# Performance work log

Measured on AMD Instinct MI355X. Metric: run time of the kernel, lower is better.

The kernel has to match this reference:

```python
import jax, jax.numpy as jnp
import numpy as np

NEG_SLOPE = 0.2
EPS = 1e-16


def _add_self_loops(edge_index, num_nodes):
    loop = jnp.arange(num_nodes, dtype=edge_index.dtype)
    return jnp.concatenate([edge_index, jnp.stack([loop, loop])], axis=1)


def gat_conv(x, edge_index, W, a_src, a_dst, b, concat):
    """PyG-style GATConv: gather -> attention logits -> segment softmax -> scatter-add."""
    N = x.shape[0]
    H, C = a_src.shape
    xl = (x @ W).reshape(N, H, C)                       # [N,H,C]
    alpha_src = (xl * a_src[None]).sum(-1)              # [N,H]
    alpha_dst = (xl * a_dst[None]).sum(-1)              # [N,H]
    src, dst = edge_index[0], edge_index[1]
    alpha = jax.nn.leaky_relu(alpha_src[src] + alpha_dst[dst], NEG_SLOPE)  # [E,H]
    amax = jax.ops.segment_max(alpha, dst, num_segments=N)
    amax = jnp.where(jnp.isfinite(amax), amax, 0.0)
    ea = jnp.exp(alpha - amax[dst])
    denom = jax.ops.segment_sum(ea, dst, num_segments=N)
    attn = ea / (denom[dst] + EPS)                      # [E,H]
    msg = xl[src] * attn[:, :, None]                    # [E,H,C]
    out = jax.ops.segment_sum(msg, dst, num_segments=N)  # [N,H,C]
    out = out.reshape(N, H * C) if concat else out.mean(axis=1)
    return out + b


def setup_inputs() -> dict:
    key = jax.random.key(0)
    ks = jax.random.split(key, 9)
    N, F, E, H, C, NC = 100000, 128, 1600000, 8, 8, 40
    s = lambda fan: 1.0 / np.sqrt(fan)
    return {
        "x": jax.random.normal(ks[0], (N, F), dtype=jnp.float32),
        "edge_index": jax.random.randint(ks[1], (2, E), 0, N, dtype=jnp.int64),
        "W1": jax.random.normal(ks[2], (F, H * C), dtype=jnp.float32) * s(F),
        "a_src1": jax.random.normal(ks[3], (H, C), dtype=jnp.float32) * s(C),
        "a_dst1": jax.random.normal(ks[4], (H, C), dtype=jnp.float32) * s(C),
        "b1": jnp.zeros((H * C,), dtype=jnp.float32),
        "W2": jax.random.normal(ks[5], (H * C, NC), dtype=jnp.float32) * s(H * C),
        "a_src2": jax.random.normal(ks[6], (1, NC), dtype=jnp.float32) * s(NC),
        "a_dst2": jax.random.normal(ks[7], (1, NC), dtype=jnp.float32) * s(NC),
        "b2": jnp.zeros((NC,), dtype=jnp.float32),
    }


def reference(x, edge_index, W1, a_src1, a_dst1, b1, W2, a_src2, a_dst2, b2):
    N = x.shape[0]
    ei = _add_self_loops(edge_index, N)
    h = gat_conv(x, ei, W1, a_src1, a_dst1, b1, concat=True)   # [N,64]
    h = jax.nn.elu(h)
    out = gat_conv(h, ei, W2, a_src2, a_dst2, b2, concat=True)  # [N,nclass]
    return out
```

## Files before the change

kernel.cpp:

```cpp
#include <hip/hip_runtime.h>
#include <math.h>

#define NEG_SLOPE 0.2f
#define GAT_EPS 1e-16f
#define LOG2E 1.44269504088896340736f

#define CH   2048
#define NBK  512
#define MAXCH 864

__device__ __forceinline__ unsigned pack_bf16(float a, float b) {
    unsigned ua = __float_as_uint(a);
    unsigned ub = __float_as_uint(b);
    ua = (ua + 0x8000u) >> 16;
    ub = (ub + 0x8000u) & 0xffff0000u;
    return ua | ub;
}
__device__ __forceinline__ float bf_lo(unsigned pk) {
    return __uint_as_float(pk << 16);
}
__device__ __forceinline__ float bf_hi(unsigned pk) {
    return __uint_as_float(pk & 0xffff0000u);
}


__global__ __launch_bounds__(256) void k_off_a(
    const int* __restrict__ cnt, int* __restrict__ off,
    int* __restrict__ tot, int NCHv)
{
    __shared__ int st[8][MAXCH];
    __shared__ int psum[8][33];
    int b0 = blockIdx.x * 8;
    int t = threadIdx.x;
    for (int idx = t; idx < NCHv * 8; idx += 256) {
        int bl = idx & 7, c = idx >> 3;
        st[bl][c] = cnt[(size_t)c * NBK + b0 + bl];
    }
    __syncthreads();
    int bl = t >> 5, j = t & 31;
    int per = (NCHv + 31) / 32;
    int cbeg = j * per;
    int cend = min(cbeg + per, NCHv);
    int s = 0;
    for (int c = cbeg; c < cend; c++) s += st[bl][c];
    psum[bl][j] = s;
    __syncthreads();
    if (j == 0) {
        int run = 0;
        for (int k = 0; k < 32; k++) { int v = psum[bl][k]; psum[bl][k] = run; run += v; }
        psum[bl][32] = run;
    }
    __syncthreads();
    int run = psum[bl][j];
    for (int c = cbeg; c < cend; c++) { int v = st[bl][c]; st[bl][c] = run; run += v; }
    __syncthreads();
    for (int idx = t; idx < NCHv * 8; idx += 256) {
        int blw = idx & 7, c = idx >> 3;
        off[(size_t)c * NBK + b0 + blw] = st[blw][c];
    }
    if (j == 0) tot[b0 + bl] = psum[bl][32];
}

__global__ __launch_bounds__(256) void k_place(
    const int* __restrict__ ei, int E, int N, int shift,
    const int* __restrict__ off, const int* __restrict__ tot,
    unsigned* __restrict__ bslab)
{
    __shared__ int cur[NBK];
    __shared__ int ps[256];
    int c = blockIdx.x;
    int t = threadIdx.x;
    int carry = 0;
    for (int b0 = 0; b0 < NBK; b0 += 256) {
        int v = tot[b0 + t];
        ps[t] = v;
        __syncthreads();
        for (int o = 1; o < 256; o <<= 1) {
            int u = (t >= o) ? ps[t - o] : 0;
            __syncthreads();
            ps[t] += u;
            __syncthreads();
        }
        cur[b0 + t] = carry + ps[t] - v + off[(size_t)c * NBK + b0 + t];
        carry += ps[255];
        __syncthreads();
    }
    __syncthreads();

    int Etot = E + N;
    int base = c * CH;
    int lim = min(base + CH, Etot);
    int mask = (1 << shift) - 1;
    for (int e = base + t; e < lim; e += 256) {
        int s, d;
        if (e < E) { s = ei[e]; d = ei[E + e]; }
        else       { s = e - E; d = s; }
        int b = d >> shift;
        int pos = atomicAdd(&cur[b], 1);
        bslab[pos] = (unsigned)s | ((unsigned)(d & mask) << 17);
    }
}

__global__ __launch_bounds__(256) void k_csr2(
    const int* __restrict__ tot, const unsigned* __restrict__ bslab,
    int shift, int* __restrict__ row_ptr, int* __restrict__ csr_src,
    int N, int Etot)
{
    __shared__ int sdeg[1024];
    __shared__ int scur[1024];
    __shared__ int ps[256];
    __shared__ int bb[NBK + 1];
    int b = blockIdx.x;
    int tid = threadIdx.x;

    int carry = 0;
    for (int b0 = 0; b0 < NBK; b0 += 256) {
        int v = tot[b0 + tid];
        ps[tid] = v;
        __syncthreads();
        for (int o = 1; o < 256; o <<= 1) {
            int u = (tid >= o) ? ps[tid - o] : 0;
            __syncthreads();
            ps[tid] += u;
            __syncthreads();
        }
        bb[b0 + tid] = carry + ps[tid] - v;
        carry += ps[255];
        __syncthreads();
    }
    if (tid == 0) bb[NBK] = carry;
    __syncthreads();

    int beg = bb[b], end = bb[b + 1];
    int nodes = 1 << shift;
    int node0 = b << shift;
    for (int i = tid; i < nodes; i += 256) sdeg[i] = 0;
    __syncthreads();
    for (int i = beg + tid; i < end; i += 256)
        atomicAdd(&sdeg[bslab[i] >> 17], 1);
    __syncthreads();
    int per = (nodes + 255) / 256;
    int mybase = tid * per;
    int sum = 0;
    for (int j = 0; j < per; j++) sum += sdeg[mybase + j];
    ps[tid] = sum;
    __syncthreads();
    int v0 = ps[tid];
    for (int o = 1; o < 256; o <<= 1) {
        int v = (tid >= o) ? ps[tid - o] : 0;
        __syncthreads();
        ps[tid] += v;
        __syncthreads();
    }
    int run = ps[tid] - v0;
    for (int j = 0; j < per; j++) {
        int i = mybase + j;
        int dgi = sdeg[i];
        scur[i] = beg + run;
        int node = node0 + i;
        if (node < N) row_ptr[node] = beg + run;
        run += dgi;
    }
    if (b == 0 && tid == 0) row_ptr[N] = Etot;
    __syncthreads();
    for (int i = beg + tid; i < end; i += 256) {
        unsigned w = bslab[i];
        int pos = atomicAdd(&scur[w >> 17], 1);
        csr_src[pos] = (int)(w & 0x1FFFFu);
    }
}

__device__ __forceinline__ void emit_node1(
    const float* acc, int n, int q, int c0,
    const float* asrc, const float* adst,
    unsigned* __restrict__ xl1b, float* __restrict__ as1,
    float* __restrict__ ad1)
{
    uint4 pk0, pk1;
    pk0.x = pack_bf16(acc[0], acc[1]);  pk0.y = pack_bf16(acc[2], acc[3]);
    pk0.z = pack_bf16(acc[4], acc[5]);  pk0.w = pack_bf16(acc[6], acc[7]);
    pk1.x = pack_bf16(acc[8], acc[9]);  pk1.y = pack_bf16(acc[10], acc[11]);
    pk1.z = pack_bf16(acc[12], acc[13]); pk1.w = pack_bf16(acc[14], acc[15]);
    uint4* xo = (uint4*)(xl1b + (size_t)n * 32 + q * 8);
    xo[0] = pk0;
    xo[1] = pk1;
#pragma unroll
    for (int hh = 0; hh < 2; hh++) {
        float s = 0.0f, t = 0.0f;
#pragma unroll
        for (int c = 0; c < 8; c++) {
            s = fmaf(acc[hh * 8 + c], asrc[c0 + hh * 8 + c], s);
            t = fmaf(acc[hh * 8 + c], adst[c0 + hh * 8 + c], t);
        }
        as1[(size_t)n * 8 + 2 * q + hh] = s * LOG2E;
        ad1[(size_t)n * 8 + 2 * q + hh] = t * LOG2E;
    }
}

__global__ __launch_bounds__(256) void k_gemm1(
    const float* __restrict__ x, const float* __restrict__ W1,
    const float* __restrict__ a_src1, const float* __restrict__ a_dst1,
    unsigned* __restrict__ xl1b, float* __restrict__ as1,
    float* __restrict__ ad1, int N, int F,
    const int* __restrict__ ei, int E, int shift, int NCHv,
    int* __restrict__ cnt)
{
    __shared__ float Ws[128 * 64];
    __shared__ float asrc[64];
    __shared__ float adst[64];
    __shared__ int hist[NBK];

    if (blockIdx.x < NCHv) {
        for (int i = threadIdx.x; i < NBK; i += 256) hist[i] = 0;
        __syncthreads();
        int Etot = E + N;
        int base = blockIdx.x * CH;
        int lim = min(base + CH, Etot);
        for (int e = base + threadIdx.x; e < lim; e += 256) {
            int d = (e < E) ? ei[E + e] : (e - E);
            atomicAdd(&hist[d >> shift], 1);
        }
        __syncthreads();
        for (int i = threadIdx.x; i < NBK; i += 256)
            cnt[(size_t)blockIdx.x * NBK + i] = hist[i];
    }
    if (blockIdx.x * 256 >= N) return;

    for (int i = threadIdx.x; i < F * 64; i += 256) Ws[i] = W1[i];
    if (threadIdx.x < 64) {
        asrc[threadIdx.x] = a_src1[threadIdx.x];
        adst[threadIdx.x] = a_dst1[threadIdx.x];
    }
    __syncthreads();

    int q = threadIdx.x & 3;
    int n0 = blockIdx.x * 256 + (threadIdx.x >> 2) * 4;
    if (n0 >= N) return;
    int c0 = q * 16;
    int n1 = min(n0 + 1, N - 1);
    int n2 = min(n0 + 2, N - 1);
    int n3 = min(n0 + 3, N - 1);

    float acc0[16], acc1[16], acc2[16], acc3[16];
#pragma unroll
    for (int c = 0; c < 16; c++) { acc0[c]=0.f; acc1[c]=0.f; acc2[c]=0.f; acc3[c]=0.f; }

    const float4* xr0 = (const float4*)(x + (size_t)n0 * F);
    const float4* xr1 = (const float4*)(x + (size_t)n1 * F);
    const float4* xr2 = (const float4*)(x + (size_t)n2 * F);
    const float4* xr3 = (const float4*)(x + (size_t)n3 * F);

#define GEMM1_ROW(comp, ridx)                                        \
    { const float* w = &Ws[(k4 * 4 + ridx) * 64 + c0];               \
      _Pragma("unroll")                                              \
      for (int c = 0; c < 16; c++) {                                 \
          float wc = w[c];                                           \
          acc0[c] = fmaf(xv0.comp, wc, acc0[c]);                     \
          acc1[c] = fmaf(xv1.comp, wc, acc1[c]);                     \
          acc2[c] = fmaf(xv2.comp, wc, acc2[c]);                     \
          acc3[c] = fmaf(xv3.comp, wc, acc3[c]); } }

    int K4 = F / 4;
    float4 xv0 = xr0[0], xv1 = xr1[0], xv2 = xr2[0], xv3 = xr3[0];
    float4 nx0 = xr0[1], nx1 = xr1[1], nx2 = xr2[1], nx3 = xr3[1];
    for (int k4 = 0; k4 < K4; k4++) {
        float4 fx0 = xv0, fx1 = xv1, fx2 = xv2, fx3 = xv3;
        int kn = k4 + 2;
        if (kn < K4) { fx0 = xr0[kn]; fx1 = xr1[kn]; fx2 = xr2[kn]; fx3 = xr3[kn]; }
        GEMM1_ROW(x, 0)
        GEMM1_ROW(y, 1)
        GEMM1_ROW(z, 2)
        GEMM1_ROW(w, 3)
        xv0 = nx0; xv1 = nx1; xv2 = nx2; xv3 = nx3;
        nx0 = fx0; nx1 = fx1; nx2 = fx2; nx3 = fx3;
    }
#undef GEMM1_ROW

    emit_node1(acc0, n0, q, c0, asrc, adst, xl1b, as1, ad1);
    if (n0 + 1 < N) emit_node1(acc1, n0 + 1, q, c0, asrc, adst, xl1b, as1, ad1);
    if (n0 + 2 < N) emit_node1(acc2, n0 + 2, q, c0, asrc, adst, xl1b, as1, ad1);
    if (n0 + 3 < N) emit_node1(acc3, n0 + 3, q, c0, asrc, adst, xl1b, as1, ad1);
}

__global__ __launch_bounds__(256) void k_agg1(
    const int* __restrict__ row_ptr, const int* __restrict__ csr_src,
    const float* __restrict__ as1, const float* __restrict__ ad1,
    const unsigned* __restrict__ xl1b, const float* __restrict__ b1,
    float* __restrict__ h1, int d0, int dend)
{
    int d = d0 + blockIdx.x * 8 + ((threadIdx.x >> 6) << 1) + ((threadIdx.x >> 5) & 1);
    if (d >= dend) return;
    int lane = threadIdx.x & 31;
    int g = lane >> 3;
    int l = lane & 7;

    int beg = row_ptr[d], end = row_ptr[d + 1];
    float adh = ad1[(size_t)d * 8 + l];

    float ax[8];
#pragma unroll
    for (int j = 0; j < 8; j++) ax[j] = 0.f;
    float den = 0.f;

    int i = beg + g;
    for (; i + 4 < end; i += 8) {
        int s0 = csr_src[i];
        int s1 = csr_src[i + 4];
        size_t q0 = (size_t)s0 * 8 + l;
        size_t q1 = (size_t)s1 * 8 + l;
        float al0 = as1[q0] + adh;
        float al1 = as1[q1] + adh;
        uint4 k0 = *(const uint4*)(xl1b + (q0 << 2));
        uint4 k1 = *(const uint4*)(xl1b + (q1 << 2));
        al0 = fmaxf(al0, NEG_SLOPE * al0);
        al1 = fmaxf(al1, NEG_SLOPE * al1);
        float e0 = __builtin_amdgcn_exp2f(al0);
        float e1 = __builtin_amdgcn_exp2f(al1);
        ax[0] = fmaf(e0, bf_lo(k0.x), ax[0]);
        ax[1] = fmaf(e0, bf_hi(k0.x), ax[1]);
        ax[2] = fmaf(e0, bf_lo(k0.y), ax[2]);
        ax[3] = fmaf(e0, bf_hi(k0.y), ax[3]);
        ax[4] = fmaf(e0, bf_lo(k0.z), ax[4]);
        ax[5] = fmaf(e0, bf_hi(k0.z), ax[5]);
        ax[6] = fmaf(e0, bf_lo(k0.w), ax[6]);
        ax[7] = fmaf(e0, bf_hi(k0.w), ax[7]);
        ax[0] = fmaf(e1, bf_lo(k1.x), ax[0]);
        ax[1] = fmaf(e1, bf_hi(k1.x), ax[1]);
        ax[2] = fmaf(e1, bf_lo(k1.y), ax[2]);
        ax[3] = fmaf(e1, bf_hi(k1.y), ax[3]);
        ax[4] = fmaf(e1, bf_lo(k1.z), ax[4]);
        ax[5] = fmaf(e1, bf_hi(k1.z), ax[5]);
        ax[6] = fmaf(e1, bf_lo(k1.w), ax[6]);
        ax[7] = fmaf(e1, bf_hi(k1.w), ax[7]);
        den += e0 + e1;
    }
    if (i < end) {
        int s0 = csr_src[i];
        size_t q0 = (size_t)s0 * 8 + l;
        float al0 = as1[q0] + adh;
        uint4 k0 = *(const uint4*)(xl1b + (q0 << 2));
        al0 = fmaxf(al0, NEG_SLOPE * al0);
        float e0 = __builtin_amdgcn_exp2f(al0);
        ax[0] = fmaf(e0, bf_lo(k0.x), ax[0]);
        ax[1] = fmaf(e0, bf_hi(k0.x), ax[1]);
        ax[2] = fmaf(e0, bf_lo(k0.y), ax[2]);
        ax[3] = fmaf(e0, bf_hi(k0.y), ax[3]);
        ax[4] = fmaf(e0, bf_lo(k0.z), ax[4]);
        ax[5] = fmaf(e0, bf_hi(k0.z), ax[5]);
        ax[6] = fmaf(e0, bf_lo(k0.w), ax[6]);
        ax[7] = fmaf(e0, bf_hi(k0.w), ax[7]);
        den += e0;
    }

#pragma unroll
    for (int m = 8; m < 32; m <<= 1) {
#pragma unroll
        for (int j = 0; j < 8; j++) ax[j] += __shfl_xor(ax[j], m);
        den += __shfl_xor(den, m);
    }

    if (g == 0) {
        float inv = __builtin_amdgcn_rcpf(den + GAT_EPS);
        const float4* bb = (const float4*)(b1 + l * 8);
        float4 b0 = bb[0], b1v = bb[1];
        float4 o0, o1;
        float v;
        v = fmaf(ax[0], inv, b0.x);  o0.x = v > 0.f ? v : __expf(v) - 1.f;
        v = fmaf(ax[1], inv, b0.y);  o0.y = v > 0.f ? v : __expf(v) - 1.f;
        v = fmaf(ax[2], inv, b0.z);  o0.z = v > 0.f ? v : __expf(v) - 1.f;
        v = fmaf(ax[3], inv, b0.w);  o0.w = v > 0.f ? v : __expf(v) - 1.f;
        v = fmaf(ax[4], inv, b1v.x); o1.x = v > 0.f ? v : __expf(v) - 1.f;
        v = fmaf(ax[5], inv, b1v.y); o1.y = v > 0.f ? v : __expf(v) - 1.f;
        v = fmaf(ax[6], inv, b1v.z); o1.z = v > 0.f ? v : __expf(v) - 1.f;
        v = fmaf(ax[7], inv, b1v.w); o1.w = v > 0.f ? v : __expf(v) - 1.f;
        float4* op = (float4*)(h1 + (size_t)d * 64 + l * 8);
        op[0] = o0;
        op[1] = o1;
    }
}

__global__ __launch_bounds__(256) void k_node2(
    const float* __restrict__ h1, const float* __restrict__ W2,
    const float* __restrict__ a_src2, const float* __restrict__ a_dst2,
    unsigned* __restrict__ xl2b, float* __restrict__ ad2, int N)
{
    __shared__ float Ws[64 * 40];
    __shared__ float a2s[40];
    __shared__ float a2d[40];
    for (int i = threadIdx.x; i < 64 * 40; i += 256) Ws[i] = W2[i];
    if (threadIdx.x < 40) {
        a2s[threadIdx.x] = a_src2[threadIdx.x];
        a2d[threadIdx.x] = a_dst2[threadIdx.x];
    }
    __syncthreads();

    int q = threadIdx.x & 1;
    int n0 = blockIdx.x * 256 + (threadIdx.x >> 1) * 2;
    if (n0 >= N) return;
    int c0 = q * 20;
    int n1 = min(n0 + 1, N - 1);

    float o0[20], o1[20];
#pragma unroll
    for (int j = 0; j < 20; j++) { o0[j] = 0.f; o1[j] = 0.f; }

    const float4* hr0 = (const float4*)(h1 + (size_t)n0 * 64);
    const float4* hr1 = (const float4*)(h1 + (size_t)n1 * 64);

#define NODE2_ROW(comp, ridx)                                        \
    { const float* w = &Ws[(k4 * 4 + ridx) * 40 + c0];               \
      _Pragma("unroll")                                              \
      for (int j = 0; j < 20; j++) {                                 \
          float wj = w[j];                                           \
          o0[j] = fmaf(ha.comp, wj, o0[j]);                          \
          o1[j] = fmaf(hb.comp, wj, o1[j]); } }

    for (int k4 = 0; k4 < 16; k4++) {
        float4 ha = hr0[k4];
        float4 hb = hr1[k4];
        NODE2_ROW(x, 0)
        NODE2_ROW(y, 1)
        NODE2_ROW(z, 2)
        NODE2_ROW(w, 3)
    }
#undef NODE2_ROW

    float s0 = 0.f, t0 = 0.f, s1 = 0.f, t1 = 0.f;
#pragma unroll
    for (int j = 0; j < 20; j++) {
        s0 = fmaf(o0[j], a2s[c0 + j], s0);
        t0 = fmaf(o0[j], a2d[c0 + j], t0);
        s1 = fmaf(o1[j], a2s[c0 + j], s1);
        t1 = fmaf(o1[j], a2d[c0 + j], t1);
    }
    s0 += __shfl_xor(s0, 1);
    t0 += __shfl_xor(t0, 1);
    s1 += __shfl_xor(s1, 1);
    t1 += __shfl_xor(t1, 1);
    if (q == 0) {
        xl2b[(size_t)n0 * 24 + 20] = __float_as_uint(s0 * LOG2E);
        ad2[n0] = t0 * LOG2E;
        if (n0 + 1 < N) {
            xl2b[(size_t)(n0 + 1) * 24 + 20] = __float_as_uint(s1 * LOG2E);
            ad2[n0 + 1] = t1 * LOG2E;
        }
    }

    unsigned* xo0 = xl2b + (size_t)n0 * 24 + q * 10;
#pragma unroll
    for (int p = 0; p < 10; p++) xo0[p] = pack_bf16(o0[2 * p], o0[2 * p + 1]);
    if (n0 + 1 < N) {
        unsigned* xo1 = xl2b + (size_t)(n0 + 1) * 24 + q * 10;
#pragma unroll
        for (int p = 0; p < 10; p++) xo1[p] = pack_bf16(o1[2 * p], o1[2 * p + 1]);
    }
}

__global__ __launch_bounds__(256) void k_agg2(
    const int* __restrict__ row_ptr, const int* __restrict__ csr_src,
    const float* __restrict__ ad2,
    const unsigned* __restrict__ xl2b, const float* __restrict__ b2,
    float* __restrict__ out, int N)
{
    int d = blockIdx.x * 8 + ((threadIdx.x >> 6) << 1) + ((threadIdx.x >> 5) & 1);
    if (d >= N) return;
    int lane = threadIdx.x & 31;
    int g = lane >> 3;
    int l = lane & 7;
    if (l >= 5) return;

    int beg = row_ptr[d], end = row_ptr[d + 1];
    float add = ad2[d];

    float ax[8];
#pragma unroll
    for (int j = 0; j < 8; j++) ax[j] = 0.f;
    float den = 0.f;

    int i = beg + g;
    for (; i + 4 < end; i += 8) {
        int s0 = csr_src[i];
        int s1 = csr_src[i + 4];
        const unsigned* r0 = xl2b + (size_t)s0 * 24;
        const unsigned* r1 = xl2b + (size_t)s1 * 24;
        float al0 = __uint_as_float(r0[20]) + add;
        float al1 = __uint_as_float(r1[20]) + add;
        uint4 k0 = *(const uint4*)(r0 + l * 4);
        uint4 k1 = *(const uint4*)(r1 + l * 4);
        al0 = fmaxf(al0, NEG_SLOPE * al0);
        al1 = fmaxf(al1, NEG_SLOPE * al1);
        float e0 = __builtin_amdgcn_exp2f(al0);
        float e1 = __builtin_amdgcn_exp2f(al1);
        ax[0] = fmaf(e0, bf_lo(k0.x), ax[0]);
        ax[1] = fmaf(e0, bf_hi(k0.x), ax[1]);
        ax[2] = fmaf(e0, bf_lo(k0.y), ax[2]);
        ax[3] = fmaf(e0, bf_hi(k0.y), ax[3]);
        ax[4] = fmaf(e0, bf_lo(k0.z), ax[4]);
        ax[5] = fmaf(e0, bf_hi(k0.z), ax[5]);
        ax[6] = fmaf(e0, bf_lo(k0.w), ax[6]);
        ax[7] = fmaf(e0, bf_hi(k0.w), ax[7]);
        ax[0] = fmaf(e1, bf_lo(k1.x), ax[0]);
        ax[1] = fmaf(e1, bf_hi(k1.x), ax[1]);
        ax[2] = fmaf(e1, bf_lo(k1.y), ax[2]);
        ax[3] = fmaf(e1, bf_hi(k1.y), ax[3]);
        ax[4] = fmaf(e1, bf_lo(k1.z), ax[4]);
        ax[5] = fmaf(e1, bf_hi(k1.z), ax[5]);
        ax[6] = fmaf(e1, bf_lo(k1.w), ax[6]);
        ax[7] = fmaf(e1, bf_hi(k1.w), ax[7]);
        den += e0 + e1;
    }
    if (i < end) {
        int s0 = csr_src[i];
        const unsigned* r0 = xl2b + (size_t)s0 * 24;
        float al0 = __uint_as_float(r0[20]) + add;
        uint4 k0 = *(const uint4*)(r0 + l * 4);
        al0 = fmaxf(al0, NEG_SLOPE * al0);
        float e0 = __builtin_amdgcn_exp2f(al0);
        ax[0] = fmaf(e0, bf_lo(k0.x), ax[0]);
        ax[1] = fmaf(e0, bf_hi(k0.x), ax[1]);
        ax[2] = fmaf(e0, bf_lo(k0.y), ax[2]);
        ax[3] = fmaf(e0, bf_hi(k0.y), ax[3]);
        ax[4] = fmaf(e0, bf_lo(k0.z), ax[4]);
        ax[5] = fmaf(e0, bf_hi(k0.z), ax[5]);
        ax[6] = fmaf(e0, bf_lo(k0.w), ax[6]);
        ax[7] = fmaf(e0, bf_hi(k0.w), ax[7]);
        den += e0;
    }

#pragma unroll
    for (int m = 8; m < 32; m <<= 1) {
#pragma unroll
        for (int j = 0; j < 8; j++) ax[j] += __shfl_xor(ax[j], m);
        den += __shfl_xor(den, m);
    }

    if (g == 0) {
        float inv = __builtin_amdgcn_rcpf(den + GAT_EPS);
        float* op = out + (size_t)d * 40 + l * 8;
        const float* bb = b2 + l * 8;
#pragma unroll
        for (int j = 0; j < 8; j++) op[j] = fmaf(ax[j], inv, bb[j]);
    }
}

extern "C" void kernel_launch(void* const* d_in, const int* in_sizes, int n_in,
                              void* d_out, int out_size, void* d_ws, size_t ws_size,
                              hipStream_t stream) {
    const float* x      = (const float*)d_in[0];
    const int*   ei     = (const int*)d_in[1];
    const float* W1     = (const float*)d_in[2];
    const float* a_src1 = (const float*)d_in[3];
    const float* a_dst1 = (const float*)d_in[4];
    const float* b1     = (const float*)d_in[5];
    const float* W2     = (const float*)d_in[6];
    const float* a_src2 = (const float*)d_in[7];
    const float* a_dst2 = (const float*)d_in[8];
    const float* b2     = (const float*)d_in[9];

    int F = in_sizes[2] / 64;
    int N = in_sizes[0] / F;
    int E = in_sizes[1] / 2;
    int Etot = E + N;
    int NCHv = (Etot + CH - 1) / CH;
    int shift = 8;
    while (((N - 1) >> shift) >= NBK) shift++;

    unsigned* xl1b    = (unsigned*)d_ws;
    float*    h1      = (float*)(xl1b + (size_t)N * 32);
    float*    as1     = h1 + (size_t)N * 64;
    float*    ad1     = as1 + (size_t)N * 8;
    int*      row_ptr = (int*)(ad1 + (size_t)N * 8);
    int*      csr_src = row_ptr + (N + 1);
    unsigned* bslab   = (unsigned*)(csr_src + Etot);
    int*      cnt     = (int*)h1;
    int*      off     = cnt + (size_t)NCHv * NBK;
    int*      tot     = off + (size_t)NCHv * NBK;
    unsigned* xl2b    = xl1b;
    float*    ad2     = ad1;

    int gridG1 = (N + 255) / 256;
    if (gridG1 < NCHv) gridG1 = NCHv;
    k_gemm1<<<gridG1, 256, 0, stream>>>(x, W1, a_src1, a_dst1,
                                        xl1b, as1, ad1, N, F,
                                        ei, E, shift, NCHv, cnt);

    k_off_a<<<NBK / 8, 256, 0, stream>>>(cnt, off, tot, NCHv);
    k_place<<<NCHv, 256, 0, stream>>>(ei, E, N, shift, off, tot, bslab);
    k_csr2 <<<NBK, 256, 0, stream>>>(tot, bslab, shift,
                                     row_ptr, csr_src, N, Etot);

    int N1 = (N / 2) & ~7;
    k_agg1 <<<(N1 + 7) / 8, 256, 0, stream>>>(row_ptr, csr_src, as1, ad1,
                                              xl1b, b1, h1, 0, N1);
    k_agg1 <<<((N - N1) + 7) / 8, 256, 0, stream>>>(row_ptr, csr_src, as1, ad1,
                                                    xl1b, b1, h1, N1, N);

    k_node2<<<(N + 255) / 256, 256, 0, stream>>>(h1, W2, a_src2, a_dst2,
                                                 xl2b, ad2, N);
    k_agg2 <<<(N + 7) / 8, 256, 0, stream>>>(row_ptr, csr_src, ad2,
                                             xl2b, b2, (float*)d_out, N);
}
```

Baseline: 302.5 us.

## Hoist bucket prefix scan into one kernel, shrink GEMM1 per-thread nodes, merge agg1 launches

Adds a single-block k_scan kernel that computes the bucket base offsets once, so k_place and k_csr2 no longer each redo a 512-entry prefix scan in every block. GEMM1 now gives each thread 2 nodes instead of 4, which doubles the grid and lowers register pressure at the cost of more W staging per node. The two split k_agg1 launches are merged into one. This adds one tiny kernel launch but removes repeated scan work and a launch.

```diff
diff --git a/kernel.cpp b/kernel.cpp
--- a/kernel.cpp
+++ b/kernel.cpp
@@ -61,30 +61,34 @@
     if (j == 0) tot[b0 + bl] = psum[bl][32];
 }
 
+__global__ __launch_bounds__(NBK) void k_scan(
+    const int* __restrict__ tot, int* __restrict__ bbase)
+{
+    __shared__ int sm[NBK];
+    int t = threadIdx.x;
+    int v = tot[t];
+    sm[t] = v;
+    __syncthreads();
+    for (int o = 1; o < NBK; o <<= 1) {
+        int u = (t >= o) ? sm[t - o] : 0;
+        __syncthreads();
+        sm[t] += u;
+        __syncthreads();
+    }
+    bbase[t] = sm[t] - v;
+    if (t == NBK - 1) bbase[NBK] = sm[t];
+}
+
 __global__ __launch_bounds__(256) void k_place(
     const int* __restrict__ ei, int E, int N, int shift,
-    const int* __restrict__ off, const int* __restrict__ tot,
+    const int* __restrict__ off, const int* __restrict__ bbase,
     unsigned* __restrict__ bslab)
 {
     __shared__ int cur[NBK];
-    __shared__ int ps[256];
     int c = blockIdx.x;
     int t = threadIdx.x;
-    int carry = 0;
-    for (int b0 = 0; b0 < NBK; b0 += 256) {
-        int v = tot[b0 + t];
-        ps[t] = v;
-        __syncthreads();
-        for (int o = 1; o < 256; o <<= 1) {
-            int u = (t >= o) ? ps[t - o] : 0;
-            __syncthreads();
-            ps[t] += u;
-            __syncthreads();
-        }
-        cur[b0 + t] = carry + ps[t] - v + off[(size_t)c * NBK + b0 + t];
-        carry += ps[255];
-        __syncthreads();
-    }
+    for (int b = t; b < NBK; b += 256)
+        cur[b] = bbase[b] + off[(size_t)c * NBK + b];
     __syncthreads();
 
     int Etot = E + N;
@@ -102,36 +106,16 @@
 }
 
 __global__ __launch_bounds__(256) void k_csr2(
-    const int* __restrict__ tot, const unsigned* __restrict__ bslab,
+    const int* __restrict__ bbase, const unsigned* __restrict__ bslab,
     int shift, int* __restrict__ row_ptr, int* __restrict__ csr_src,
     int N, int Etot)
 {
     __shared__ int sdeg[1024];
     __shared__ int scur[1024];
     __shared__ int ps[256];
-    __shared__ int bb[NBK + 1];
     int b = blockIdx.x;
     int tid = threadIdx.x;
-
-    int carry = 0;
-    for (int b0 = 0; b0 < NBK; b0 += 256) {
-        int v = tot[b0 + tid];
-        ps[tid] = v;
-        __syncthreads();
-        for (int o = 1; o < 256; o <<= 1) {
-            int u = (tid >= o) ? ps[tid - o] : 0;
-            __syncthreads();
-            ps[tid] += u;
-            __syncthreads();
-        }
-        bb[b0 + tid] = carry + ps[tid] - v;
-        carry += ps[255];
-        __syncthreads();
-    }
-    if (tid == 0) bb[NBK] = carry;
-    __syncthreads();
-
-    int beg = bb[b], end = bb[b + 1];
+    int beg = bbase[b], end = bbase[b + 1];
     int nodes = 1 << shift;
     int node0 = b << shift;
     for (int i = tid; i < nodes; i += 256) sdeg[i] = 0;
@@ -224,7 +208,7 @@
         for (int i = threadIdx.x; i < NBK; i += 256)
             cnt[(size_t)blockIdx.x * NBK + i] = hist[i];
     }
-    if (blockIdx.x * 256 >= N) return;
+    if (blockIdx.x * 128 >= N) return;
 
     for (int i = threadIdx.x; i < F * 64; i += 256) Ws[i] = W1[i];
     if (threadIdx.x < 64) {
@@ -234,21 +218,17 @@
     __syncthreads();
 
     int q = threadIdx.x & 3;
-    int n0 = blockIdx.x * 256 + (threadIdx.x >> 2) * 4;
+    int n0 = blockIdx.x * 128 + (threadIdx.x >> 2) * 2;
     if (n0 >= N) return;
     int c0 = q * 16;
     int n1 = min(n0 + 1, N - 1);
-    int n2 = min(n0 + 2, N - 1);
-    int n3 = min(n0 + 3, N - 1);
-
-    float acc0[16], acc1[16], acc2[16], acc3[16];
-#pragma unroll
-    for (int c = 0; c < 16; c++) { acc0[c]=0.f; acc1[c]=0.f; acc2[c]=0.f; acc3[c]=0.f; }
+
+    float acc0[16], acc1[16];
+#pragma unroll
+    for (int c = 0; c < 16; c++) { acc0[c] = 0.f; acc1[c] = 0.f; }
 
     const float4* xr0 = (const float4*)(x + (size_t)n0 * F);
     const float4* xr1 = (const float4*)(x + (size_t)n1 * F);
-    const float4* xr2 = (const float4*)(x + (size_t)n2 * F);
-    const float4* xr3 = (const float4*)(x + (size_t)n3 * F);
 
 #define GEMM1_ROW(comp, ridx)                                        \
     { const float* w = &Ws[(k4 * 4 + ridx) * 64 + c0];               \
@@ -256,40 +236,36 @@
       for (int c = 0; c < 16; c++) {                                 \
           float wc = w[c];                                           \
           acc0[c] = fmaf(xv0.comp, wc, acc0[c]);                     \
-          acc1[c] = fmaf(xv1.comp, wc, acc1[c]);                     \
-          acc2[c] = fmaf(xv2.comp, wc, acc2[c]);                     \
-          acc3[c] = fmaf(xv3.comp, wc, acc3[c]); } }
+          acc1[c] = fmaf(xv1.comp, wc, acc1[c]); } }
 
     int K4 = F / 4;
-    float4 xv0 = xr0[0], xv1 = xr1[0], xv2 = xr2[0], xv3 = xr3[0];
-    float4 nx0 = xr0[1], nx1 = xr1[1], nx2 = xr2[1], nx3 = xr3[1];
+    float4 xv0 = xr0[0], xv1 = xr1[0];
+    float4 nx0 = xr0[1], nx1 = xr1[1];
     for (int k4 = 0; k4 < K4; k4++) {
-        float4 fx0 = xv0, fx1 = xv1, fx2 = xv2, fx3 = xv3;
+        float4 fx0 = xv0, fx1 = xv1;
         int kn = k4 + 2;
-        if (kn < K4) { fx0 = xr0[kn]; fx1 = xr1[kn]; fx2 = xr2[kn]; fx3 = xr3[kn]; }
+        if (kn < K4) { fx0 = xr0[kn]; fx1 = xr1[kn]; }
         GEMM1_ROW(x, 0)
         GEMM1_ROW(y, 1)
         GEMM1_ROW(z, 2)
         GEMM1_ROW(w, 3)
-        xv0 = nx0; xv1 = nx1; xv2 = nx2; xv3 = nx3;
-        nx0 = fx0; nx1 = fx1; nx2 = fx2; nx3 = fx3;
+        xv0 = nx0; xv1 = nx1;
+        nx0 = fx0; nx1 = fx1;
     }
 #undef GEMM1_ROW
 
     emit_node1(acc0, n0, q, c0, asrc, adst, xl1b, as1, ad1);
     if (n0 + 1 < N) emit_node1(acc1, n0 + 1, q, c0, asrc, adst, xl1b, as1, ad1);
-    if (n0 + 2 < N) emit_node1(acc2, n0 + 2, q, c0, asrc, adst, xl1b, as1, ad1);
-    if (n0 + 3 < N) emit_node1(acc3, n0 + 3, q, c0, asrc, adst, xl1b, as1, ad1);
 }
 
 __global__ __launch_bounds__(256) void k_agg1(
     const int* __restrict__ row_ptr, const int* __restrict__ csr_src,
     const float* __restrict__ as1, const float* __restrict__ ad1,
     const unsigned* __restrict__ xl1b, const float* __restrict__ b1,
-    float* __restrict__ h1, int d0, int dend)
-{
-    int d = d0 + blockIdx.x * 8 + ((threadIdx.x >> 6) << 1) + ((threadIdx.x >> 5) & 1);
-    if (d >= dend) return;
+    float* __restrict__ h1, int N)
+{
+    int d = blockIdx.x * 8 + ((threadIdx.x >> 6) << 1) + ((threadIdx.x >> 5) & 1);
+    if (d >= N) return;
     int lane = threadIdx.x & 31;
     int g = lane >> 3;
     int l = lane & 7;
@@ -575,25 +551,24 @@
     int*      cnt     = (int*)h1;
     int*      off     = cnt + (size_t)NCHv * NBK;
     int*      tot     = off + (size_t)NCHv * NBK;
+    int*      bbase   = tot + NBK;
     unsigned* xl2b    = xl1b;
     float*    ad2     = ad1;
 
-    int gridG1 = (N + 255) / 256;
+    int gridG1 = (N + 127) / 128;
     if (gridG1 < NCHv) gridG1 = NCHv;
     k_gemm1<<<gridG1, 256, 0, stream>>>(x, W1, a_src1, a_dst1,
                                         xl1b, as1, ad1, N, F,
                                         ei, E, shift, NCHv, cnt);
 
     k_off_a<<<NBK / 8, 256, 0, stream>>>(cnt, off, tot, NCHv);
-    k_place<<<NCHv, 256, 0, stream>>>(ei, E, N, shift, off, tot, bslab);
-    k_csr2 <<<NBK, 256, 0, stream>>>(tot, bslab, shift,
+    k_scan <<<1, NBK, 0, stream>>>(tot, bbase);
+    k_place<<<NCHv, 256, 0, stream>>>(ei, E, N, shift, off, bbase, bslab);
+    k_csr2 <<<NBK, 256, 0, stream>>>(bbase, bslab, shift,
                                      row_ptr, csr_src, N, Etot);
 
-    int N1 = (N / 2) & ~7;
-    k_agg1 <<<(N1 + 7) / 8, 256, 0, stream>>>(row_ptr, csr_src, as1, ad1,
-                                              xl1b, b1, h1, 0, N1);
-    k_agg1 <<<((N - N1) + 7) / 8, 256, 0, stream>>>(row_ptr, csr_src, as1, ad1,
-                                                    xl1b, b1, h1, N1, N);
+    k_agg1 <<<(N + 7) / 8, 256, 0, stream>>>(row_ptr, csr_src, as1, ad1,
+                                             xl1b, b1, h1, N);
 
     k_node2<<<(N + 255) / 256, 256, 0, stream>>>(h1, W2, a_src2, a_dst2,
                                                  xl2b, ad2, N);
```

Measured after the change: 297.9 us. No clear change (-1.5%).
